# Performance work log

Hardware: AMD Instinct MI355X
Metric: run time of the kernel (lower is better)

Reference implementation:

```python
import jax, jax.numpy as jnp
import numpy as np

N = 43
H = N // 2  # 21


def _mk(key, i, o):
    kw, kb = jax.random.split(key)
    bound = 1.0 / np.sqrt(i)
    W = jax.random.uniform(kw, (i, o), jnp.float32, -bound, bound)
    b = jax.random.uniform(kb, (o,), jnp.float32, -bound, bound)
    return W, b


def setup_inputs() -> dict:
    key = jax.random.key(0)
    keys = jax.random.split(key, 11)
    x = jax.random.normal(keys[0], (1048576, N), jnp.float32)
    dims = [(N, N), (N, N), (N, N), (N, N), (N, H),  # encoder
            (H, N), (N, N), (N, N), (N, N), (N, N)]  # decoder
    out = {"x": x}
    for li, (i, o) in enumerate(dims):
        W, b = _mk(keys[li + 1], i, o)
        out[f"W{li}"] = W
        out[f"b{li}"] = b
    return out


def reference(x, W0, b0, W1, b1, W2, b2, W3, b3, W4, b4,
              W5, b5, W6, b6, W7, b7, W8, b8, W9, b9):
    Ws = [W0, W1, W2, W3, W4, W5, W6, W7, W8, W9]
    bs = [b0, b1, b2, b3, b4, b5, b6, b7, b8, b9]
    h = x
    for li in range(10):
        h = h @ Ws[li] + bs[li]
        # tanh after every layer except encoder bottleneck (4) and final (9)
        if li not in (4, 9):
            h = jnp.tanh(h)
    return h
```

## Files before the change

kernel.cpp:

```cpp
#include <hip/hip_runtime.h>


typedef __fp16 pk16x2 __attribute__((ext_vector_type(2)));
typedef _Float16 f16x8 __attribute__((ext_vector_type(8)));
typedef float f32x4 __attribute__((ext_vector_type(4)));

#define TPB 1024
#define NBLK 256
#define ITERS 8
#define NROWS 1048576
#define NCOL 43
#define ROWB 172u
#define XBYTES (NROWS * (size_t)ROWB)
#define WSTRIDE 72
#define WSLOT (48 * WSTRIDE)
#define W_BYTES (10 * WSLOT * 2)
#define HBUF_HW (32 * WSTRIDE)
#define HBUF_BYTES (HBUF_HW * 2)
#define H_BASE W_BYTES
#define SMEM_BYTES (H_BASE + 16 * HBUF_BYTES)

__device__ __forceinline__ float fast_tanh(float x) {
  float t = __builtin_amdgcn_exp2f(x * 2.8853900817779268f);
  float r = __builtin_amdgcn_rcpf(t + 1.0f);
  return __builtin_fmaf(-2.0f, r, 1.0f);
}

__device__ __forceinline__ void store_h4(_Float16* dst, float v0, float v1,
                                         float v2, float v3) {
  union { pk16x2 h[2]; uint2 u; } p;
  p.h[0] = __builtin_amdgcn_cvt_pkrtz(v0, v1);
  p.h[1] = __builtin_amdgcn_cvt_pkrtz(v2, v3);
  *(uint2*)dst = p.u;
}

template <int NT, int KC, bool DOTANH, int NLOUT>
__device__ __forceinline__ void mid_layer(const _Float16* __restrict__ Wl,
                                          _Float16* Hw, int g, int lr) {
  f16x8 Bv[2][KC];
#pragma unroll
  for (int s = 0; s < 2; ++s)
#pragma unroll
    for (int c = 0; c < KC; ++c)
      Bv[s][c] = *(const f16x8*)(Hw + (16 * s + lr) * WSTRIDE + 8 * g + 32 * c);

  f32x4 acc[NT][2];
#pragma unroll
  for (int t = 0; t < NT; ++t)
#pragma unroll
    for (int s = 0; s < 2; ++s) acc[t][s] = f32x4{0.f, 0.f, 0.f, 0.f};

#pragma unroll
  for (int c = 0; c < KC; ++c)
#pragma unroll
    for (int t = 0; t < NT; ++t) {
      f16x8 A = *(const f16x8*)(Wl + (16 * t + lr) * WSTRIDE + 8 * g + 32 * c);
#pragma unroll
      for (int s = 0; s < 2; ++s)
        acc[t][s] = __builtin_amdgcn_mfma_f32_16x16x32_f16(A, Bv[s][c],
                                                           acc[t][s], 0, 0, 0);
    }

#pragma unroll
  for (int t = 0; t < NT; ++t)
#pragma unroll
    for (int s = 0; s < 2; ++s) {
      float v[4];
#pragma unroll
      for (int r = 0; r < 4; ++r) {
        int col = 16 * t + 4 * g + r;
        float u = acc[t][s][r];
        if (DOTANH) u = fast_tanh(u);
        v[r] = (col < NLOUT) ? u : ((col == NLOUT) ? 1.0f : 0.0f);
      }
      store_h4(Hw + (16 * s + lr) * WSTRIDE + 16 * t + 4 * g,
               v[0], v[1], v[2], v[3]);
    }
}

extern "C" __global__ void __launch_bounds__(TPB, 1)
ae_kernel(const float* __restrict__ x,
          const float* __restrict__ W0, const float* __restrict__ B0,
          const float* __restrict__ W1, const float* __restrict__ B1,
          const float* __restrict__ W2, const float* __restrict__ B2,
          const float* __restrict__ W3, const float* __restrict__ B3,
          const float* __restrict__ W4, const float* __restrict__ B4,
          const float* __restrict__ W5, const float* __restrict__ B5,
          const float* __restrict__ W6, const float* __restrict__ B6,
          const float* __restrict__ W7, const float* __restrict__ B7,
          const float* __restrict__ W8, const float* __restrict__ B8,
          const float* __restrict__ W9, const float* __restrict__ B9,
          float* __restrict__ out) {
  extern __shared__ char smem[];
  _Float16* lw = (_Float16*)smem;

  const int tid = threadIdx.x;
  const int wave = tid >> 6;
  const int lane = tid & 63;
  const int g = lane >> 4;
  const int lr = lane & 15;

  {
    const float* Wp[10] = {W0, W1, W2, W3, W4, W5, W6, W7, W8, W9};
    const float* Bp[10] = {B0, B1, B2, B3, B4, B5, B6, B7, B8, B9};
    const int KLs[10] = {43, 43, 43, 43, 43, 21, 43, 43, 43, 43};
    const int NLs[10] = {43, 43, 43, 43, 21, 43, 43, 43, 43, 43};
#pragma unroll
    for (int L = 0; L < 10; ++L) {
      const float* Wl = Wp[L];
      const float* Bl = Bp[L];
      const int KL = KLs[L], NL = NLs[L];
      for (int idx = tid; idx < 48 * 64; idx += TPB) {
        int n = idx >> 6, k = idx & 63;
        float v = 0.0f;
        if (n < NL) {
          if (k < KL) v = Wl[k * NL + n];
          else if (k == KL && L != 0) v = Bl[n];
        }
        lw[L * WSLOT + n * WSTRIDE + k] = (_Float16)v;
      }
    }
  }

  _Float16* Hw = (_Float16*)(smem + H_BASE + wave * HBUF_BYTES);

  {
    unsigned* h32 = (unsigned*)Hw;
#pragma unroll
    for (int i = 0; i < 18; ++i) h32[lane + 64 * i] = 0;
  }

  float b0v[12];
#pragma unroll
  for (int t = 0; t < 3; ++t)
#pragma unroll
    for (int r = 0; r < 4; ++r) {
      int n = 16 * t + 4 * g + r;
      b0v[t * 4 + r] = (n < NCOL) ? B0[n] : 0.0f;
    }

  pk16x2 m1[4];
#pragma unroll
  for (int j2 = 0; j2 < 4; ++j2) {
    m1[j2][0] = (__fp16)((32 + 8 * g + 2 * j2 + 0 < NCOL) ? 1.0f : 0.0f);
    m1[j2][1] = (__fp16)((32 + 8 * g + 2 * j2 + 1 < NCOL) ? 1.0f : 0.0f);
  }

  __syncthreads();

  const char* xc = (const char*)x;
  const unsigned blockbase = (unsigned)blockIdx.x * (ITERS * 512) + wave * 32;
  const unsigned LIM = (unsigned)(XBYTES - 4);

  float xv0[2][8], xv1[2][8];
#pragma unroll
  for (int s = 0; s < 2; ++s) {
    unsigned rb = (blockbase + 16 * s + lr) * ROWB;
    unsigned a0 = rb + 32u * g;
    unsigned a1 = rb + 128u + 32u * g;
#pragma unroll
    for (int j = 0; j < 8; ++j) {
      xv0[s][j] = *(const float*)(xc + (a0 + 4u * j));
      unsigned a = a1 + 4u * j;
      xv1[s][j] = *(const float*)(xc + (a < LIM ? a : LIM));
    }
  }

#pragma unroll 1
  for (int it = 0; it < ITERS; ++it) {
    const unsigned row0 = blockbase + (unsigned)it * 512u;

    f16x8 Bv[2][2];
#pragma unroll
    for (int s = 0; s < 2; ++s) {
      union { pk16x2 h[4]; f16x8 v; } u0, u1;
#pragma unroll
      for (int j2 = 0; j2 < 4; ++j2) {
        u0.h[j2] = __builtin_amdgcn_cvt_pkrtz(xv0[s][2 * j2], xv0[s][2 * j2 + 1]);
        u1.h[j2] = __builtin_amdgcn_cvt_pkrtz(xv1[s][2 * j2], xv1[s][2 * j2 + 1])
                   * m1[j2];
      }
      Bv[s][0] = u0.v;
      Bv[s][1] = u1.v;
    }

    if (it + 1 < ITERS) {
#pragma unroll
      for (int s = 0; s < 2; ++s) {
        unsigned rb = (row0 + 512u + 16 * s + lr) * ROWB;
        unsigned a0 = rb + 32u * g;
        unsigned a1 = rb + 128u + 32u * g;
#pragma unroll
        for (int j = 0; j < 8; ++j) {
          xv0[s][j] = *(const float*)(xc + (a0 + 4u * j));
          unsigned a = a1 + 4u * j;
          xv1[s][j] = *(const float*)(xc + (a < LIM ? a : LIM));
        }
      }
    }

    f32x4 acc[3][2];
#pragma unroll
    for (int t = 0; t < 3; ++t)
#pragma unroll
      for (int s = 0; s < 2; ++s) acc[t][s] = f32x4{0.f, 0.f, 0.f, 0.f};
#pragma unroll
    for (int c = 0; c < 2; ++c)
#pragma unroll
      for (int t = 0; t < 3; ++t) {
        f16x8 A = *(const f16x8*)(lw + (16 * t + lr) * WSTRIDE + 8 * g + 32 * c);
#pragma unroll
        for (int s = 0; s < 2; ++s)
          acc[t][s] = __builtin_amdgcn_mfma_f32_16x16x32_f16(A, Bv[s][c],
                                                             acc[t][s], 0, 0, 0);
      }
#pragma unroll
    for (int t = 0; t < 3; ++t)
#pragma unroll
      for (int s = 0; s < 2; ++s) {
        float v[4];
#pragma unroll
        for (int r = 0; r < 4; ++r) {
          int col = 16 * t + 4 * g + r;
          float u = fast_tanh(acc[t][s][r] + b0v[t * 4 + r]);
          v[r] = (col < NCOL) ? u : ((col == NCOL) ? 1.0f : 0.0f);
        }
        store_h4(Hw + (16 * s + lr) * WSTRIDE + 16 * t + 4 * g,
                 v[0], v[1], v[2], v[3]);
      }

    mid_layer<3, 2, true, 43>(lw + 1 * WSLOT, Hw, g, lr);
    mid_layer<3, 2, true, 43>(lw + 2 * WSLOT, Hw, g, lr);
    mid_layer<3, 2, true, 43>(lw + 3 * WSLOT, Hw, g, lr);
    mid_layer<2, 2, false, 21>(lw + 4 * WSLOT, Hw, g, lr);
    mid_layer<3, 1, true, 43>(lw + 5 * WSLOT, Hw, g, lr);
    mid_layer<3, 2, true, 43>(lw + 6 * WSLOT, Hw, g, lr);
    mid_layer<3, 2, true, 43>(lw + 7 * WSLOT, Hw, g, lr);
    mid_layer<3, 2, true, 43>(lw + 8 * WSLOT, Hw, g, lr);

    {
      f16x8 B9[2][2];
#pragma unroll
      for (int s = 0; s < 2; ++s)
#pragma unroll
        for (int c = 0; c < 2; ++c)
          B9[s][c] = *(const f16x8*)(Hw + (16 * s + lr) * WSTRIDE + 8 * g + 32 * c);
      f32x4 a9[3][2];
#pragma unroll
      for (int t = 0; t < 3; ++t)
#pragma unroll
        for (int s = 0; s < 2; ++s) a9[t][s] = f32x4{0.f, 0.f, 0.f, 0.f};
#pragma unroll
      for (int c = 0; c < 2; ++c)
#pragma unroll
        for (int t = 0; t < 3; ++t) {
          f16x8 A = *(const f16x8*)(lw + 9 * WSLOT + (16 * t + lr) * WSTRIDE +
                                    8 * g + 32 * c);
#pragma unroll
          for (int s = 0; s < 2; ++s)
            a9[t][s] = __builtin_amdgcn_mfma_f32_16x16x32_f16(A, B9[s][c],
                                                              a9[t][s], 0, 0, 0);
        }
#pragma unroll
      for (int t = 0; t < 3; ++t)
#pragma unroll
        for (int s = 0; s < 2; ++s)
#pragma unroll
          for (int r = 0; r < 4; ++r) {
            int col = 16 * t + 4 * g + r;
            if (col < NCOL)
              out[(size_t)(row0 + 16 * s + lr) * NCOL + col] = a9[t][s][r];
          }
    }
  }
}

extern "C" void kernel_launch(void* const* d_in, const int* in_sizes, int n_in,
                              void* d_out, int out_size, void* d_ws,
                              size_t ws_size, hipStream_t stream) {
  const float* x = (const float*)d_in[0];
  const float* W[10];
  const float* B[10];
  for (int i = 0; i < 10; ++i) {
    W[i] = (const float*)d_in[1 + 2 * i];
    B[i] = (const float*)d_in[2 + 2 * i];
  }
  (void)hipFuncSetAttribute(reinterpret_cast<const void*>(ae_kernel),
                            hipFuncAttributeMaxDynamicSharedMemorySize,
                            SMEM_BYTES);
  ae_kernel<<<dim3(NBLK), dim3(TPB), SMEM_BYTES, stream>>>(
      x, W[0], B[0], W[1], B[1], W[2], B[2], W[3], B[3], W[4], B[4],
      W[5], B[5], W[6], B[6], W[7], B[7], W[8], B[8], W[9], B[9],
      (float*)d_out);
}
```

Baseline: 159.9 us.

## Keep layer activations in registers by permuting weight K layout

Activations no longer round-trip through a per-wave LDS buffer between layers. The MFMA accumulator output is packed directly into the B-operand fragments for the next layer. To make that possible, the K dimension of each stored weight matrix is permuted so its order matches the accumulator's register order. This removes the LDS stores and loads between the ten layers and the buffer zeroing. In exchange it adds register pressure and some index-permutation complexity in the weight setup.

```diff
diff --git a/kernel.cpp b/kernel.cpp
--- a/kernel.cpp
+++ b/kernel.cpp
@@ -14,11 +14,7 @@
 #define XBYTES (NROWS * (size_t)ROWB)
 #define WSTRIDE 72
 #define WSLOT (48 * WSTRIDE)
-#define W_BYTES (10 * WSLOT * 2)
-#define HBUF_HW (32 * WSTRIDE)
-#define HBUF_BYTES (HBUF_HW * 2)
-#define H_BASE W_BYTES
-#define SMEM_BYTES (H_BASE + 16 * HBUF_BYTES)
+#define SMEM_BYTES (10 * WSLOT * 2)
 
 __device__ __forceinline__ float fast_tanh(float x) {
   float t = __builtin_amdgcn_exp2f(x * 2.8853900817779268f);
@@ -26,30 +22,62 @@
   return __builtin_fmaf(-2.0f, r, 1.0f);
 }
 
-__device__ __forceinline__ void store_h4(_Float16* dst, float v0, float v1,
-                                         float v2, float v3) {
-  union { pk16x2 h[2]; uint2 u; } p;
-  p.h[0] = __builtin_amdgcn_cvt_pkrtz(v0, v1);
-  p.h[1] = __builtin_amdgcn_cvt_pkrtz(v2, v3);
-  *(uint2*)dst = p.u;
-}
-
-template <int NT, int KC, bool DOTANH, int NLOUT>
-__device__ __forceinline__ void mid_layer(const _Float16* __restrict__ Wl,
-                                          _Float16* Hw, int g, int lr) {
-  f16x8 Bv[2][KC];
-#pragma unroll
-  for (int s = 0; s < 2; ++s)
-#pragma unroll
-    for (int c = 0; c < KC; ++c)
-      Bv[s][c] = *(const f16x8*)(Hw + (16 * s + lr) * WSTRIDE + 8 * g + 32 * c);
-
-  f32x4 acc[NT][2];
+__device__ __forceinline__ unsigned pk2(float a, float b) {
+  pk16x2 h = __builtin_amdgcn_cvt_pkrtz(a, b);
+  return __builtin_bit_cast(unsigned, h);
+}
+
+struct Frags { f16x8 b[2][2]; };
+
+template <int NT, bool DOTANH, int NLOUT, int KCN, bool ADDB>
+__device__ __forceinline__ Frags epi_pack(f32x4 acc[3][2],
+                                          const float* badd, int g) {
+  Frags O;
+#pragma unroll
+  for (int s = 0; s < 2; ++s) {
+    unsigned pk[3][2];
+#pragma unroll
+    for (int t = 0; t < NT; ++t) {
+      float v[4];
+#pragma unroll
+      for (int r = 0; r < 4; ++r) {
+        float u = acc[t][s][r];
+        if (ADDB) u += badd[t * 4 + r];
+        if (DOTANH) u = fast_tanh(u);
+        if (t == (NLOUT >> 4)) {
+          int col = 16 * t + 4 * g + r;
+          u = (col == NLOUT) ? 1.0f : u;
+        }
+        v[r] = u;
+      }
+      pk[t][0] = pk2(v[0], v[1]);
+      pk[t][1] = pk2(v[2], v[3]);
+    }
+    union { unsigned d[4]; f16x8 v; } u0;
+    u0.d[0] = pk[0][0]; u0.d[1] = pk[0][1];
+    u0.d[2] = pk[1][0]; u0.d[3] = pk[1][1];
+    O.b[s][0] = u0.v;
+    if (KCN == 2) {
+      union { unsigned d[4]; f16x8 v; } u1;
+      u1.d[0] = pk[2][0]; u1.d[1] = pk[2][1];
+      u1.d[2] = 0u;       u1.d[3] = 0u;
+      O.b[s][1] = u1.v;
+    } else {
+      O.b[s][1] = O.b[s][0];
+    }
+  }
+  return O;
+}
+
+template <int NT, int KC, bool DOTANH, int NLOUT, int KCN, bool ADDB>
+__device__ __forceinline__ Frags layer_fwd(const _Float16* __restrict__ Wl,
+                                           const Frags& B, const float* badd,
+                                           int g, int lr) {
+  f32x4 acc[3][2];
 #pragma unroll
   for (int t = 0; t < NT; ++t)
 #pragma unroll
     for (int s = 0; s < 2; ++s) acc[t][s] = f32x4{0.f, 0.f, 0.f, 0.f};
-
 #pragma unroll
   for (int c = 0; c < KC; ++c)
 #pragma unroll
@@ -57,25 +85,10 @@
       f16x8 A = *(const f16x8*)(Wl + (16 * t + lr) * WSTRIDE + 8 * g + 32 * c);
 #pragma unroll
       for (int s = 0; s < 2; ++s)
-        acc[t][s] = __builtin_amdgcn_mfma_f32_16x16x32_f16(A, Bv[s][c],
+        acc[t][s] = __builtin_amdgcn_mfma_f32_16x16x32_f16(A, B.b[s][c],
                                                            acc[t][s], 0, 0, 0);
     }
-
-#pragma unroll
-  for (int t = 0; t < NT; ++t)
-#pragma unroll
-    for (int s = 0; s < 2; ++s) {
-      float v[4];
-#pragma unroll
-      for (int r = 0; r < 4; ++r) {
-        int col = 16 * t + 4 * g + r;
-        float u = acc[t][s][r];
-        if (DOTANH) u = fast_tanh(u);
-        v[r] = (col < NLOUT) ? u : ((col == NLOUT) ? 1.0f : 0.0f);
-      }
-      store_h4(Hw + (16 * s + lr) * WSTRIDE + 16 * t + 4 * g,
-               v[0], v[1], v[2], v[3]);
-    }
+  return epi_pack<NT, DOTANH, NLOUT, KCN, ADDB>(acc, badd, g);
 }
 
 extern "C" __global__ void __launch_bounds__(TPB, 1)
@@ -111,23 +124,22 @@
       const float* Bl = Bp[L];
       const int KL = KLs[L], NL = NLs[L];
       for (int idx = tid; idx < 48 * 64; idx += TPB) {
-        int n = idx >> 6, k = idx & 63;
+        int n = idx >> 6, kp = idx & 63;
         float v = 0.0f;
         if (n < NL) {
-          if (k < KL) v = Wl[k * NL + n];
-          else if (k == KL && L != 0) v = Bl[n];
-        }
-        lw[L * WSLOT + n * WSTRIDE + k] = (_Float16)v;
-      }
-    }
-  }
-
-  _Float16* Hw = (_Float16*)(smem + H_BASE + wave * HBUF_BYTES);
-
-  {
-    unsigned* h32 = (unsigned*)Hw;
-#pragma unroll
-    for (int i = 0; i < 18; ++i) h32[lane + 64 * i] = 0;
+          int c = kp >> 5, g2 = (kp >> 3) & 3, j = kp & 7;
+          int d = j >> 1, o = j & 1;
+          int F;
+          if (L == 0) F = kp;
+          else if (c == 0) F = 16 * (d >> 1) + 4 * g2 + 2 * (d & 1) + o;
+          else if (d < 2)  F = 32 + 4 * g2 + 2 * d + o;
+          else             F = 63;
+          if (F < KL) v = Wl[F * NL + n];
+          else if (F == KL && L != 0) v = Bl[n];
+        }
+        lw[L * WSLOT + n * WSTRIDE + kp] = (_Float16)v;
+      }
+    }
   }
 
   float b0v[12];
@@ -139,13 +151,6 @@
       b0v[t * 4 + r] = (n < NCOL) ? B0[n] : 0.0f;
     }
 
-  pk16x2 m1[4];
-#pragma unroll
-  for (int j2 = 0; j2 < 4; ++j2) {
-    m1[j2][0] = (__fp16)((32 + 8 * g + 2 * j2 + 0 < NCOL) ? 1.0f : 0.0f);
-    m1[j2][1] = (__fp16)((32 + 8 * g + 2 * j2 + 1 < NCOL) ? 1.0f : 0.0f);
-  }
-
   __syncthreads();
 
   const char* xc = (const char*)x;
@@ -156,12 +161,10 @@
 #pragma unroll
   for (int s = 0; s < 2; ++s) {
     unsigned rb = (blockbase + 16 * s + lr) * ROWB;
-    unsigned a0 = rb + 32u * g;
-    unsigned a1 = rb + 128u + 32u * g;
 #pragma unroll
     for (int j = 0; j < 8; ++j) {
-      xv0[s][j] = *(const float*)(xc + (a0 + 4u * j));
-      unsigned a = a1 + 4u * j;
+      xv0[s][j] = *(const float*)(xc + (rb + 32u * g + 4u * j));
+      unsigned a = rb + 128u + 32u * g + 4u * j;
       xv1[s][j] = *(const float*)(xc + (a < LIM ? a : LIM));
     }
   }
@@ -170,81 +173,43 @@
   for (int it = 0; it < ITERS; ++it) {
     const unsigned row0 = blockbase + (unsigned)it * 512u;
 
-    f16x8 Bv[2][2];
+    Frags B;
 #pragma unroll
     for (int s = 0; s < 2; ++s) {
-      union { pk16x2 h[4]; f16x8 v; } u0, u1;
+      union { unsigned d[4]; f16x8 v; } u0, u1;
 #pragma unroll
       for (int j2 = 0; j2 < 4; ++j2) {
-        u0.h[j2] = __builtin_amdgcn_cvt_pkrtz(xv0[s][2 * j2], xv0[s][2 * j2 + 1]);
-        u1.h[j2] = __builtin_amdgcn_cvt_pkrtz(xv1[s][2 * j2], xv1[s][2 * j2 + 1])
-                   * m1[j2];
-      }
-      Bv[s][0] = u0.v;
-      Bv[s][1] = u1.v;
+        u0.d[j2] = pk2(xv0[s][2 * j2], xv0[s][2 * j2 + 1]);
+        u1.d[j2] = pk2(xv1[s][2 * j2], xv1[s][2 * j2 + 1]);
+      }
+      B.b[s][0] = u0.v;
+      B.b[s][1] = u1.v;
     }
 
     if (it + 1 < ITERS) {
 #pragma unroll
       for (int s = 0; s < 2; ++s) {
         unsigned rb = (row0 + 512u + 16 * s + lr) * ROWB;
-        unsigned a0 = rb + 32u * g;
-        unsigned a1 = rb + 128u + 32u * g;
 #pragma unroll
         for (int j = 0; j < 8; ++j) {
-          xv0[s][j] = *(const float*)(xc + (a0 + 4u * j));
-          unsigned a = a1 + 4u * j;
+          xv0[s][j] = *(const float*)(xc + (rb + 32u * g + 4u * j));
+          unsigned a = rb + 128u + 32u * g + 4u * j;
           xv1[s][j] = *(const float*)(xc + (a < LIM ? a : LIM));
         }
       }
     }
 
-    f32x4 acc[3][2];
-#pragma unroll
-    for (int t = 0; t < 3; ++t)
-#pragma unroll
-      for (int s = 0; s < 2; ++s) acc[t][s] = f32x4{0.f, 0.f, 0.f, 0.f};
-#pragma unroll
-    for (int c = 0; c < 2; ++c)
-#pragma unroll
-      for (int t = 0; t < 3; ++t) {
-        f16x8 A = *(const f16x8*)(lw + (16 * t + lr) * WSTRIDE + 8 * g + 32 * c);
-#pragma unroll
-        for (int s = 0; s < 2; ++s)
-          acc[t][s] = __builtin_amdgcn_mfma_f32_16x16x32_f16(A, Bv[s][c],
-                                                             acc[t][s], 0, 0, 0);
-      }
-#pragma unroll
-    for (int t = 0; t < 3; ++t)
-#pragma unroll
-      for (int s = 0; s < 2; ++s) {
-        float v[4];
-#pragma unroll
-        for (int r = 0; r < 4; ++r) {
-          int col = 16 * t + 4 * g + r;
-          float u = fast_tanh(acc[t][s][r] + b0v[t * 4 + r]);
-          v[r] = (col < NCOL) ? u : ((col == NCOL) ? 1.0f : 0.0f);
-        }
-        store_h4(Hw + (16 * s + lr) * WSTRIDE + 16 * t + 4 * g,
-                 v[0], v[1], v[2], v[3]);
-      }
-
-    mid_layer<3, 2, true, 43>(lw + 1 * WSLOT, Hw, g, lr);
-    mid_layer<3, 2, true, 43>(lw + 2 * WSLOT, Hw, g, lr);
-    mid_layer<3, 2, true, 43>(lw + 3 * WSLOT, Hw, g, lr);
-    mid_layer<2, 2, false, 21>(lw + 4 * WSLOT, Hw, g, lr);
-    mid_layer<3, 1, true, 43>(lw + 5 * WSLOT, Hw, g, lr);
-    mid_layer<3, 2, true, 43>(lw + 6 * WSLOT, Hw, g, lr);
-    mid_layer<3, 2, true, 43>(lw + 7 * WSLOT, Hw, g, lr);
-    mid_layer<3, 2, true, 43>(lw + 8 * WSLOT, Hw, g, lr);
+    B = layer_fwd<3, 2, true, 43, 2, true >(lw + 0 * WSLOT, B, b0v, g, lr);
+    B = layer_fwd<3, 2, true, 43, 2, false>(lw + 1 * WSLOT, B, nullptr, g, lr);
+    B = layer_fwd<3, 2, true, 43, 2, false>(lw + 2 * WSLOT, B, nullptr, g, lr);
+    B = layer_fwd<3, 2, true, 43, 2, false>(lw + 3 * WSLOT, B, nullptr, g, lr);
+    B = layer_fwd<2, 2, false, 21, 1, false>(lw + 4 * WSLOT, B, nullptr, g, lr);
+    B = layer_fwd<3, 1, true, 43, 2, false>(lw + 5 * WSLOT, B, nullptr, g, lr);
+    B = layer_fwd<3, 2, true, 43, 2, false>(lw + 6 * WSLOT, B, nullptr, g, lr);
+    B = layer_fwd<3, 2, true, 43, 2, false>(lw + 7 * WSLOT, B, nullptr, g, lr);
+    B = layer_fwd<3, 2, true, 43, 2, false>(lw + 8 * WSLOT, B, nullptr, g, lr);
 
     {
-      f16x8 B9[2][2];
-#pragma unroll
-      for (int s = 0; s < 2; ++s)
-#pragma unroll
-        for (int c = 0; c < 2; ++c)
-          B9[s][c] = *(const f16x8*)(Hw + (16 * s + lr) * WSTRIDE + 8 * g + 32 * c);
       f32x4 a9[3][2];
 #pragma unroll
       for (int t = 0; t < 3; ++t)
@@ -258,7 +223,7 @@
                                     8 * g + 32 * c);
 #pragma unroll
           for (int s = 0; s < 2; ++s)
-            a9[t][s] = __builtin_amdgcn_mfma_f32_16x16x32_f16(A, B9[s][c],
+            a9[t][s] = __builtin_amdgcn_mfma_f32_16x16x32_f16(A, B.b[s][c],
                                                               a9[t][s], 0, 0, 0);
         }
 #pragma unroll
```

Result: slower. 538.6 us (+236.9%).
